# Kernel optimization log

Measured on AMD Instinct MI355X. Metric: run time of the kernel, lower is better.

Reference implementation:

```python
import jax, jax.numpy as jnp
from jax import lax
import numpy as np

D_MODEL, D_STATE, D_CONV, D_INNER = 1024, 16, 4, 2048
BATCH, SEQ = 2, 2048


def setup_inputs() -> dict:
    key = jax.random.key(0)
    ks = jax.random.split(key, 7)
    s = lambda fan: 1.0 / np.sqrt(fan)
    return {
        "x": jax.random.normal(ks[0], (BATCH, SEQ, D_MODEL), jnp.float32),
        "W_in": jax.random.normal(ks[1], (2 * D_INNER, D_MODEL), jnp.float32) * s(D_MODEL),
        "conv_w": jax.random.normal(ks[2], (D_INNER, 1, D_CONV), jnp.float32) * s(D_CONV),
        "conv_b": jax.random.normal(ks[3], (D_INNER,), jnp.float32) * 0.02,
        "A_log": jax.random.normal(ks[4], (D_INNER, D_STATE), jnp.float32),
        "W_x": jax.random.normal(ks[5], (2 * D_STATE + 1, D_INNER), jnp.float32) * s(D_INNER),
        "W_out": jax.random.normal(ks[6], (D_MODEL, D_INNER), jnp.float32) * s(D_INNER),
    }


def reference(x, W_in, conv_w, conv_b, A_log, W_x, W_out):
    B, L, _ = x.shape
    di, ds = D_INNER, D_STATE

    # in_proj and chunk into (x_proj, z)
    xz = jnp.einsum("bld,ed->ble", x, W_in)          # [B, L, 2*di]
    xp, z = xz[..., :di], xz[..., di:]

    # depthwise causal conv1d: padding = d_conv-1 on left, then trim to L
    xc = jnp.transpose(xp, (0, 2, 1))                 # [B, di, L]
    xc = lax.conv_general_dilated(
        xc, conv_w, window_strides=(1,), padding=[(D_CONV - 1, 0)],
        feature_group_count=di)
    xc = xc + conv_b[None, :, None]
    xc = jnp.transpose(xc, (0, 2, 1))                 # [B, L, di]
    xc = jax.nn.silu(xc)

    A = -jnp.exp(A_log.astype(jnp.float32))           # [di, ds]

    # input-dependent delta, B, C
    xdbl = jnp.einsum("bld,ed->ble", xc, W_x)         # [B, L, 2*ds+1]
    delta = jax.nn.softplus(xdbl[..., :1])            # [B, L, 1]
    Bm = xdbl[..., 1:1 + ds]                          # [B, L, ds]
    Cm = xdbl[..., 1 + ds:]                           # [B, L, ds]

    # selective scan: h_t = exp(delta_t * A) * h_{t-1} + delta_t * B_t (outer) u_t
    def step(h, inp):
        d_t, b_t, c_t, u_t = inp                      # [B,1], [B,ds], [B,ds], [B,di]
        dA = jnp.exp(d_t[:, :, None] * A[None])       # [B, di, ds]
        h = dA * h + d_t[:, :, None] * b_t[:, None, :] * u_t[:, :, None]
        y_t = jnp.einsum("bds,bs->bd", h, c_t)        # [B, di]
        return h, y_t

    h0 = jnp.zeros((B, di, ds), xc.dtype)
    inps = (jnp.swapaxes(delta, 0, 1), jnp.swapaxes(Bm, 0, 1),
            jnp.swapaxes(Cm, 0, 1), jnp.swapaxes(xc, 0, 1))
    _, ys = lax.scan(step, h0, inps)                  # ys: [L, B, di]
    y = jnp.swapaxes(ys, 0, 1)                        # [B, L, di]

    y = y * jax.nn.silu(z)
    return jnp.einsum("bld,ed->ble", y, W_out)        # [B, L, d_model]
```

## Files before the change

### kernel.cpp

```cpp
#include <hip/hip_runtime.h>

#define DM    1024
#define DS    16
#define DI    2048
#define LSEQ  2048
#define BL    4096
#define NC    64
#define CHK   32

typedef float          f32x4  __attribute__((ext_vector_type(4)));
typedef float          f32x16 __attribute__((ext_vector_type(16)));
typedef unsigned int   u32x4  __attribute__((ext_vector_type(4)));
typedef unsigned short u16x8  __attribute__((ext_vector_type(8)));

__device__ __forceinline__ unsigned short f2bf(float f) {
    unsigned int u = __float_as_uint(f);
    u += 0x7fffu + ((u >> 16) & 1u);
    return (unsigned short)(u >> 16);
}

__device__ __forceinline__ float bf2f(unsigned short u) {
    return __uint_as_float((unsigned int)u << 16);
}

__device__ __forceinline__ float silu_f(float x) {
    return x / (1.f + __expf(-x));
}

__device__ __forceinline__ void mfma_bf16(f32x4& d, const u32x4& a, const u32x4& b) {
    asm("v_mfma_f32_16x16x32_bf16 %0, %1, %2, %0" : "+v"(d) : "v"(a), "v"(b));
}

__device__ __forceinline__ void gload16(const void* g, void* l) {
    __builtin_amdgcn_global_load_lds(
        (const __attribute__((address_space(1))) unsigned int*)g,
        (__attribute__((address_space(3))) unsigned int*)l, 16, 0, 0);
}

__global__ __launch_bounds__(256) void cvt_bf16_kernel(const float* __restrict__ in,
                                                       unsigned short* __restrict__ out,
                                                       int n) {
    int i = blockIdx.x * 256 + threadIdx.x;
    if (i < n) out[i] = f2bf(in[i]);
}

__global__ __launch_bounds__(256) void wx_pad_kernel(const float* __restrict__ Wx,
                                                     unsigned short* __restrict__ out) {
    int i = blockIdx.x * 256 + threadIdx.x;
    int e = i >> 11;
    out[i] = (e < 33) ? f2bf(Wx[i]) : (unsigned short)0;
}

template <int NF, typename OUT>
__global__ __launch_bounds__(256) void gemm_bf16_nt(const unsigned short* __restrict__ A,
                                                    const unsigned short* __restrict__ B,
                                                    OUT* __restrict__ C,
                                                    int M, int N, int K, int KS) {
    constexpr int BN = NF * 32;
    __shared__ unsigned short As[2][128 * 32];
    __shared__ unsigned short Bs[2][BN * 32];

    const int tid  = threadIdx.x;
    const int lane = tid & 63;
    const int wave = tid >> 6;
    const int wr = wave >> 1, wc = wave & 1;
    const int lrow = lane & 15, lkh = lane >> 4;

    const long m0 = (long)blockIdx.y * 128;
    const long n0 = (long)blockIdx.x * BN;
    const int koff = blockIdx.z * KS;

    const int scb = ((tid & 3) ^ ((tid >> 3) & 3)) * 8;
    const unsigned short* pa = A + (m0 + (tid >> 2)) * K + koff + scb;
    const unsigned short* pb = B + (n0 + (tid >> 2)) * K + koff + scb;
    const long half = (long)64 * K;

    OUT* Cz = C + (long)blockIdx.z * M * (long)N;

    const int swa = (lrow >> 1) & 3;

    f32x4 acc[4][NF];
#pragma unroll
    for (int i = 0; i < 4; ++i)
#pragma unroll
        for (int j = 0; j < NF; ++j)
            acc[i][j] = (f32x4){0.f, 0.f, 0.f, 0.f};

    auto STAGE = [&](int buf, int k0) {
        char* a = (char*)&As[buf][0] + wave * 1024;
        gload16(pa + k0,        a);
        gload16(pa + half + k0, a + 4096);
        char* b = (char*)&Bs[buf][0] + wave * 1024;
        gload16(pb + k0, b);
        if constexpr (NF == 4) gload16(pb + half + k0, b + 4096);
    };

    STAGE(0, 0);
    asm volatile("s_waitcnt vmcnt(0)" ::: "memory");
    __builtin_amdgcn_s_barrier();
    __builtin_amdgcn_sched_barrier(0);

    int cur = 0;
    for (int k0 = 0; k0 < KS; k0 += 32) {
        const bool notlast = (k0 + 32 < KS);
        if (notlast) STAGE(cur ^ 1, k0 + 32);

        u32x4 af[4], bfr[NF];
#pragma unroll
        for (int i = 0; i < 4; ++i)
            af[i] = *(const u32x4*)(&As[cur][(wr * 64 + i * 16 + lrow) * 32 + ((lkh ^ swa) * 8)]);
#pragma unroll
        for (int j = 0; j < NF; ++j)
            bfr[j] = *(const u32x4*)(&Bs[cur][(wc * NF * 16 + j * 16 + lrow) * 32 + ((lkh ^ swa) * 8)]);

        __builtin_amdgcn_s_setprio(1);
#pragma unroll
        for (int i = 0; i < 4; ++i)
#pragma unroll
            for (int j = 0; j < NF; ++j)
                mfma_bf16(acc[i][j], af[i], bfr[j]);
        __builtin_amdgcn_s_setprio(0);

        if (notlast) {
            asm volatile("s_waitcnt vmcnt(0)" ::: "memory");
            __builtin_amdgcn_s_barrier();
            __builtin_amdgcn_sched_barrier(0);
            cur ^= 1;
        }
    }

    asm volatile("s_nop 7\n\ts_nop 7" ::: "memory");

#pragma unroll
    for (int i = 0; i < 4; ++i)
#pragma unroll
        for (int j = 0; j < NF; ++j)
#pragma unroll
            for (int r = 0; r < 4; ++r) {
                long row = m0 + wr * 64 + i * 16 + lkh * 4 + r;
                long col = n0 + wc * NF * 16 + j * 16 + lrow;
                float v = acc[i][j][r];
                if constexpr (sizeof(OUT) == 2) Cz[row * (long)N + col] = f2bf(v);
                else                            Cz[row * (long)N + col] = v;
            }
}

__global__ __launch_bounds__(256) void conv_silu_kernel(const unsigned short* __restrict__ xzbf,
                                                        const float* __restrict__ cw,
                                                        const float* __restrict__ cb,
                                                        unsigned short* __restrict__ xcbf) {
    int idx = blockIdx.x * 256 + threadIdx.x;
    int d8 = (idx & 255) * 8;
    int m  = idx >> 8;
    int t  = m & (LSEQ - 1);
    const unsigned short* p = xzbf + (long)m * (2 * DI) + d8;
    u16x8 tap0 = (u16x8)(0), tap1 = (u16x8)(0), tap2 = (u16x8)(0);
    u16x8 tap3 = *(const u16x8*)(p);
    if (t >= 1) tap2 = *(const u16x8*)(p - 1 * 2 * DI);
    if (t >= 2) tap1 = *(const u16x8*)(p - 2 * 2 * DI);
    if (t >= 3) tap0 = *(const u16x8*)(p - 3 * 2 * DI);

    u16x8 o;
#pragma unroll
    for (int k = 0; k < 8; ++k) {
        const float4 wv = *(const float4*)(cw + 4 * (d8 + k));
        float s = cb[d8 + k];
        s = fmaf(bf2f(tap0[k]), wv.x, s);
        s = fmaf(bf2f(tap1[k]), wv.y, s);
        s = fmaf(bf2f(tap2[k]), wv.z, s);
        s = fmaf(bf2f(tap3[k]), wv.w, s);
        o[k] = f2bf(silu_f(s));
    }
    *(u16x8*)(xcbf + (long)m * DI + d8) = o;
}

__global__ __launch_bounds__(256) void xdbl_reduce_kernel(const float* __restrict__ part,
                                                          float* __restrict__ dlt,
                                                          float* __restrict__ BC) {
    int idx = blockIdx.x * 256 + threadIdx.x;
    if (idx >= BL * 33) return;
    int m = idx / 33;
    int j = idx - m * 33;
    float v = 0.f;
#pragma unroll
    for (int g = 0; g < 8; ++g) v += part[(long)g * (BL * 128) + (long)m * 128 + j];
    if (j == 0) dlt[m] = (v > 20.f) ? v : log1pf(expf(v));
    else        BC[(long)m * 32 + (j - 1)] = v;
}

__global__ __launch_bounds__(256) void scan_pass1(const float* __restrict__ dlt,
                                                  const float* __restrict__ BC,
                                                  const unsigned short* __restrict__ xcbf,
                                                  const float* __restrict__ A_log,
                                                  float* __restrict__ P_,
                                                  float* __restrict__ S_) {
    __shared__ float sdl[CHK];
    __shared__ float sbc[CHK * 32];

    const int tid = threadIdx.x;
    const int c   = blockIdx.x;
    const int ch  = blockIdx.y * 256 + tid;
    const int b   = ch >> 11;
    const int d   = ch & (DI - 1);
    const long m0 = (long)b * LSEQ + (long)c * CHK;

    *(float4*)(sbc + tid * 4) = *(const float4*)(BC + m0 * 32 + tid * 4);
    if (tid < CHK) sdl[tid] = dlt[m0 + tid];

    f32x16 A, h, P;
#pragma unroll
    for (int s = 0; s < 16; ++s) {
        A[s] = -__expf(A_log[d * 16 + s]);
        h[s] = 0.f;
        P[s] = 1.f;
    }
    const unsigned short* ur = xcbf + m0 * DI + d;
    __syncthreads();

    for (int t = 0; t < CHK; ++t) {
        float dl = sdl[t];
        float u  = bf2f(ur[(long)t * DI]);
        float du = dl * u;
#pragma unroll
        for (int q = 0; q < 4; ++q) {
            f32x4 bq = *(const f32x4*)(sbc + t * 32 + q * 4);
#pragma unroll
            for (int j = 0; j < 4; ++j) {
                const int s = q * 4 + j;
                float dA = __expf(dl * A[s]);
                P[s] *= dA;
                h[s] = fmaf(dA, h[s], du * bq[j]);
            }
        }
    }
    float* pp = P_ + ((long)c * 4096 + ch) * 16;
    float* sp = S_ + ((long)c * 4096 + ch) * 16;
#pragma unroll
    for (int q = 0; q < 4; ++q) {
        *(f32x4*)(pp + q * 4) = (f32x4){P[q*4], P[q*4+1], P[q*4+2], P[q*4+3]};
        *(f32x4*)(sp + q * 4) = (f32x4){h[q*4], h[q*4+1], h[q*4+2], h[q*4+3]};
    }
}

__global__ __launch_bounds__(256) void scan_pass2(const float* __restrict__ P_,
                                                  float* __restrict__ S_) {
    const long idx = (long)blockIdx.x * 256 + threadIdx.x;
    float h = 0.f;
    for (int c0 = 0; c0 < NC; c0 += 8) {
        float p[8], s[8];
#pragma unroll
        for (int i = 0; i < 8; ++i) {
            p[i] = P_[(long)(c0 + i) * 65536 + idx];
            s[i] = S_[(long)(c0 + i) * 65536 + idx];
        }
#pragma unroll
        for (int i = 0; i < 8; ++i) {
            S_[(long)(c0 + i) * 65536 + idx] = h;
            h = fmaf(p[i], h, s[i]);
        }
    }
}

__global__ __launch_bounds__(256) void scan_pass3(const float* __restrict__ dlt,
                                                  const float* __restrict__ BC,
                                                  const unsigned short* __restrict__ xcbf,
                                                  const unsigned short* __restrict__ xzbf,
                                                  const float* __restrict__ A_log,
                                                  const float* __restrict__ H0,
                                                  unsigned short* __restrict__ ybf) {
    __shared__ float sdl[CHK];
    __shared__ float sbc[CHK * 32];

    const int tid = threadIdx.x;
    const int c   = blockIdx.x;
    const int ch  = blockIdx.y * 256 + tid;
    const int b   = ch >> 11;
    const int d   = ch & (DI - 1);
    const long m0 = (long)b * LSEQ + (long)c * CHK;

    *(float4*)(sbc + tid * 4) = *(const float4*)(BC + m0 * 32 + tid * 4);
    if (tid < CHK) sdl[tid] = dlt[m0 + tid];

    f32x16 A, h;
    const float* h0p = H0 + ((long)c * 4096 + ch) * 16;
    {
        f32x4 h0a = *(const f32x4*)(h0p + 0);
        f32x4 h0b = *(const f32x4*)(h0p + 4);
        f32x4 h0c = *(const f32x4*)(h0p + 8);
        f32x4 h0d = *(const f32x4*)(h0p + 12);
#pragma unroll
        for (int j = 0; j < 4; ++j) {
            h[j]      = h0a[j];
            h[4 + j]  = h0b[j];
            h[8 + j]  = h0c[j];
            h[12 + j] = h0d[j];
        }
    }
#pragma unroll
    for (int s = 0; s < 16; ++s) A[s] = -__expf(A_log[d * 16 + s]);

    const unsigned short* ur = xcbf + m0 * DI + d;
    const unsigned short* zr = xzbf + m0 * (2 * DI) + DI + d;
    unsigned short* yr = ybf + m0 * DI + d;
    __syncthreads();

    for (int t = 0; t < CHK; ++t) {
        float dl = sdl[t];
        float u  = bf2f(ur[(long)t * DI]);
        float z  = bf2f(zr[(long)t * 2 * DI]);
        float du = dl * u;
        float y = 0.f;
#pragma unroll
        for (int q = 0; q < 4; ++q) {
            f32x4 bq = *(const f32x4*)(sbc + t * 32 + q * 4);
            f32x4 cq = *(const f32x4*)(sbc + t * 32 + 16 + q * 4);
#pragma unroll
            for (int j = 0; j < 4; ++j) {
                const int s = q * 4 + j;
                float dA = __expf(dl * A[s]);
                h[s] = fmaf(dA, h[s], du * bq[j]);
                y = fmaf(h[s], cq[j], y);
            }
        }
        yr[(long)t * DI] = f2bf(y * silu_f(z));
    }
}

extern "C" void kernel_launch(void* const* d_in, const int* in_sizes, int n_in,
                              void* d_out, int out_size, void* d_ws, size_t ws_size,
                              hipStream_t stream) {
    const float* x      = (const float*)d_in[0];
    const float* W_in   = (const float*)d_in[1];
    const float* conv_w = (const float*)d_in[2];
    const float* conv_b = (const float*)d_in[3];
    const float* A_log  = (const float*)d_in[4];
    const float* W_x    = (const float*)d_in[5];
    const float* W_out  = (const float*)d_in[6];
    float* out = (float*)d_out;

    char* w = (char*)d_ws;
    unsigned short* xbf  = (unsigned short*)(w + 0);
    unsigned short* wbf  = (unsigned short*)(w + 8388608);
    unsigned short* xzbf = (unsigned short*)(w + 16777216);
    unsigned short* xcbf = (unsigned short*)(w + 50331648);
    float*          dlt  = (float*)(w + 67108864);
    float*          BC   = (float*)(w + 67125248);
    float*          P_   = (float*)(w + 67649536);
    float*          S_   = (float*)(w + 84426752);

    unsigned short* wobf      = xbf;
    unsigned short* wxbf      = (unsigned short*)(w + 8388608);
    float*          xdbl_part = (float*)P_;
    unsigned short* ybf       = (unsigned short*)P_;

    cvt_bf16_kernel<<<dim3(16384), dim3(256), 0, stream>>>(x, xbf, BL * DM);
    cvt_bf16_kernel<<<dim3(16384), dim3(256), 0, stream>>>(W_in, wbf, 2 * DI * DM);
    gemm_bf16_nt<4, unsigned short><<<dim3(32, 32, 1), dim3(256), 0, stream>>>(xbf, wbf, xzbf, BL, 2 * DI, DM, DM);
    cvt_bf16_kernel<<<dim3(8192), dim3(256), 0, stream>>>(W_out, wobf, DM * DI);
    wx_pad_kernel<<<dim3(1024), dim3(256), 0, stream>>>(W_x, wxbf);
    conv_silu_kernel<<<dim3((BL * DI / 8) / 256), dim3(256), 0, stream>>>(xzbf, conv_w, conv_b, xcbf);
    gemm_bf16_nt<4, float><<<dim3(1, 32, 8), dim3(256), 0, stream>>>(xcbf, wxbf, xdbl_part, BL, 128, DI, 256);
    xdbl_reduce_kernel<<<dim3(528), dim3(256), 0, stream>>>(xdbl_part, dlt, BC);
    scan_pass1<<<dim3(NC, 16), dim3(256), 0, stream>>>(dlt, BC, xcbf, A_log, P_, S_);
    scan_pass2<<<dim3(256), dim3(256), 0, stream>>>(P_, S_);
    scan_pass3<<<dim3(NC, 16), dim3(256), 0, stream>>>(dlt, BC, xcbf, xzbf, A_log, S_, ybf);
    gemm_bf16_nt<2, float><<<dim3(16, 32, 1), dim3(256), 0, stream>>>(ybf, wobf, out, BL, DM, DI, DI);
}
```

Before: 226.9 us.

## Use 256x256 four-stage pipelined GEMM for in_proj and fuse bf16 conversion kernels

Replaces the in_proj GEMM with a new 256x256-tile, 512-thread kernel that uses a four-buffer LDS pipeline, swizzled LDS layout, explicit waitcnt scheduling and setprio around the MFMA blocks. It also merges the four fp32-to-bf16 conversion launches into two vectorized float4 kernels. The goal is more data reuse per tile, better overlap of loads with MFMA, and fewer launches. The cost is a large LDS footprint and high register pressure, plus a grid of only 256 blocks, which may leave part of the GPU underused.

```diff
diff --git a/kernel.cpp b/kernel.cpp
--- a/kernel.cpp
+++ b/kernel.cpp
@@ -37,18 +37,150 @@
         (__attribute__((address_space(3))) unsigned int*)l, 16, 0, 0);
 }
 
-__global__ __launch_bounds__(256) void cvt_bf16_kernel(const float* __restrict__ in,
-                                                       unsigned short* __restrict__ out,
-                                                       int n) {
+__global__ __launch_bounds__(256) void prep_inputs_kernel(const float* __restrict__ x,
+                                                          const float* __restrict__ W_in,
+                                                          unsigned short* __restrict__ xbf,
+                                                          unsigned short* __restrict__ wbf) {
+    const int n4 = (BL * DM) / 4;
     int i = blockIdx.x * 256 + threadIdx.x;
-    if (i < n) out[i] = f2bf(in[i]);
-}
-
-__global__ __launch_bounds__(256) void wx_pad_kernel(const float* __restrict__ Wx,
-                                                     unsigned short* __restrict__ out) {
+    const float* src = (i < n4) ? x : W_in;
+    unsigned short* dst = (i < n4) ? xbf : wbf;
+    int j = (i < n4) ? i : i - n4;
+    float4 v = *(const float4*)(src + j * 4);
+    ushort4 o;
+    o.x = f2bf(v.x); o.y = f2bf(v.y); o.z = f2bf(v.z); o.w = f2bf(v.w);
+    *(ushort4*)(dst + j * 4) = o;
+}
+
+__global__ __launch_bounds__(256) void prep_weights_kernel(const float* __restrict__ W_out,
+                                                           const float* __restrict__ Wx,
+                                                           unsigned short* __restrict__ wobf,
+                                                           unsigned short* __restrict__ wxbf) {
+    const int n4 = (DM * DI) / 4;
     int i = blockIdx.x * 256 + threadIdx.x;
-    int e = i >> 11;
-    out[i] = (e < 33) ? f2bf(Wx[i]) : (unsigned short)0;
+    if (i < n4) {
+        float4 v = *(const float4*)(W_out + i * 4);
+        ushort4 o;
+        o.x = f2bf(v.x); o.y = f2bf(v.y); o.z = f2bf(v.z); o.w = f2bf(v.w);
+        *(ushort4*)(wobf + i * 4) = o;
+    } else {
+        int j = i - n4;
+        if (j < 128 * 2048) {
+            int e = j >> 11;
+            wxbf[j] = (e < 33) ? f2bf(Wx[j]) : (unsigned short)0;
+        }
+    }
+}
+
+template <typename OUT>
+__global__ __launch_bounds__(512, 2) void gemm256_bf16_nt(const unsigned short* __restrict__ A,
+                                                          const unsigned short* __restrict__ B,
+                                                          OUT* __restrict__ C,
+                                                          int M, int N, int K) {
+    __shared__ unsigned short As[4][256 * 32];
+    __shared__ unsigned short Bs[4][256 * 32];
+
+    const int tid  = threadIdx.x;
+    const int lane = tid & 63;
+    const int wave = tid >> 6;
+    const int wm = wave >> 2;
+    const int wn = wave & 3;
+    const int lrow = lane & 15, lkh = lane >> 4;
+    const int swa  = (lrow >> 1) & 3;
+
+    const long m0 = (long)blockIdx.y * 256;
+    const long n0 = (long)blockIdx.x * 256;
+
+    const int scb = ((tid & 3) ^ ((tid >> 3) & 3)) * 8;
+    const unsigned short* pa = A + (m0 + (tid >> 2)) * K + scb;
+    const unsigned short* pb = B + (n0 + (tid >> 2)) * K + scb;
+    const long rstep = (long)128 * K;
+
+    const int NT = K >> 5;
+
+    f32x4 acc[8][4];
+#pragma unroll
+    for (int i = 0; i < 8; ++i)
+#pragma unroll
+        for (int j = 0; j < 4; ++j)
+            acc[i][j] = (f32x4){0.f, 0.f, 0.f, 0.f};
+
+#define STAGE_A(t) { char* d_ = (char*)&As[(t) & 3][0] + wave * 1024;          \
+                     gload16(pa + (long)(t) * 32,         d_);                 \
+                     gload16(pa + rstep + (long)(t) * 32, d_ + 8192); }
+#define STAGE_B(t) { char* d_ = (char*)&Bs[(t) & 3][0] + wave * 1024;          \
+                     gload16(pb + (long)(t) * 32,         d_);                 \
+                     gload16(pb + rstep + (long)(t) * 32, d_ + 8192); }
+
+    STAGE_A(0); STAGE_B(0);
+    STAGE_A(1); STAGE_B(1);
+    STAGE_A(2); STAGE_B(2);
+    asm volatile("s_waitcnt vmcnt(8)" ::: "memory");
+    __builtin_amdgcn_s_barrier();
+    __builtin_amdgcn_sched_barrier(0);
+
+    for (int t = 0; t < NT; ++t) {
+        const unsigned short* as = &As[t & 3][0];
+        const unsigned short* bs = &Bs[t & 3][0];
+        const bool st = (t + 3 < NT);
+
+        u32x4 af[4], bfr[4];
+#pragma unroll
+        for (int j = 0; j < 4; ++j)
+            bfr[j] = *(const u32x4*)(bs + (wn * 64 + j * 16 + lrow) * 32 + ((lkh ^ swa) * 8));
+#pragma unroll
+        for (int i = 0; i < 4; ++i)
+            af[i] = *(const u32x4*)(as + (wm * 128 + i * 16 + lrow) * 32 + ((lkh ^ swa) * 8));
+        if (st) STAGE_A(t + 3);
+        asm volatile("s_waitcnt lgkmcnt(0)" ::: "memory");
+        __builtin_amdgcn_sched_barrier(0);
+        __builtin_amdgcn_s_setprio(1);
+#pragma unroll
+        for (int i = 0; i < 4; ++i)
+#pragma unroll
+            for (int j = 0; j < 4; ++j)
+                mfma_bf16(acc[i][j], af[i], bfr[j]);
+        __builtin_amdgcn_s_setprio(0);
+
+#pragma unroll
+        for (int i = 0; i < 4; ++i)
+            af[i] = *(const u32x4*)(as + (wm * 128 + (i + 4) * 16 + lrow) * 32 + ((lkh ^ swa) * 8));
+        if (st) STAGE_B(t + 3);
+        asm volatile("s_waitcnt lgkmcnt(0)" ::: "memory");
+        __builtin_amdgcn_sched_barrier(0);
+        __builtin_amdgcn_s_setprio(1);
+#pragma unroll
+        for (int i = 0; i < 4; ++i)
+#pragma unroll
+            for (int j = 0; j < 4; ++j)
+                mfma_bf16(acc[i + 4][j], af[i], bfr[j]);
+        __builtin_amdgcn_s_setprio(0);
+
+        if (t < NT - 1) {
+            if (t <= NT - 4)      asm volatile("s_waitcnt vmcnt(8)" ::: "memory");
+            else if (t == NT - 3) asm volatile("s_waitcnt vmcnt(4)" ::: "memory");
+            else                  asm volatile("s_waitcnt vmcnt(0)" ::: "memory");
+            __builtin_amdgcn_s_barrier();
+            __builtin_amdgcn_sched_barrier(0);
+        }
+    }
+#undef STAGE_A
+#undef STAGE_B
+
+    asm volatile("s_nop 7\n\ts_nop 7" ::: "memory");
+
+#pragma unroll
+    for (int i = 0; i < 8; ++i)
+#pragma unroll
+        for (int j = 0; j < 4; ++j)
+#pragma unroll
+            for (int r = 0; r < 4; ++r) {
+                long row = m0 + wm * 128 + i * 16 + lkh * 4 + r;
+                long col = n0 + wn * 64 + j * 16 + lrow;
+                float v = acc[i][j][r];
+                if constexpr (sizeof(OUT) == 2) C[row * (long)N + col] = f2bf(v);
+                else                            C[row * (long)N + col] = v;
+            }
 }
 
 template <int NF, typename OUT>
@@ -353,11 +485,9 @@
     float*          xdbl_part = (float*)P_;
     unsigned short* ybf       = (unsigned short*)P_;
 
-    cvt_bf16_kernel<<<dim3(16384), dim3(256), 0, stream>>>(x, xbf, BL * DM);
-    cvt_bf16_kernel<<<dim3(16384), dim3(256), 0, stream>>>(W_in, wbf, 2 * DI * DM);
-    gemm_bf16_nt<4, unsigned short><<<dim3(32, 32, 1), dim3(256), 0, stream>>>(xbf, wbf, xzbf, BL, 2 * DI, DM, DM);
-    cvt_bf16_kernel<<<dim3(8192), dim3(256), 0, stream>>>(W_out, wobf, DM * DI);
-    wx_pad_kernel<<<dim3(1024), dim3(256), 0, stream>>>(W_x, wxbf);
+    prep_inputs_kernel<<<dim3(8192), dim3(256), 0, stream>>>(x, W_in, xbf, wbf);
+    gemm256_bf16_nt<unsigned short><<<dim3(16, 16), dim3(512), 0, stream>>>(xbf, wbf, xzbf, BL, 2 * DI, DM);
+    prep_weights_kernel<<<dim3(3072), dim3(256), 0, stream>>>(W_out, W_x, wobf, wxbf);
     conv_silu_kernel<<<dim3((BL * DI / 8) / 256), dim3(256), 0, stream>>>(xzbf, conv_w, conv_b, xcbf);
     gemm_bf16_nt<4, float><<<dim3(1, 32, 8), dim3(256), 0, stream>>>(xcbf, wxbf, xdbl_part, BL, 128, DI, 256);
     xdbl_reduce_kernel<<<dim3(528), dim3(256), 0, stream>>>(xdbl_part, dlt, BC);
```

Result: faster. 214.2 us (-5.6%).
